# Kernel tuning notes

Hardware: AMD Instinct MI355X
Metric: run time of the kernel (lower is better)

The kernel has to match this reference:

```python
import jax, jax.numpy as jnp
import numpy as np

C1, C2, BIG_K, STRIDE = 256, 256, 13, 1
EPS = 1e-5  # BatchNorm2d default


def setup_inputs() -> dict:
    key = jax.random.key(0)
    k1, k2, k3, k4, k5 = jax.random.split(key, 5)
    x = jax.random.normal(k1, (16, C1, 56, 56), dtype=jnp.float32)
    # Conv2d weight: (out_ch, in_ch, kH, kW), kaiming-ish scale
    w = jax.random.normal(k2, (C2, C1, BIG_K, BIG_K), dtype=jnp.float32) * (1.0 / np.sqrt(C1 * BIG_K * BIG_K))
    gamma = jax.random.uniform(k3, (C2,), dtype=jnp.float32, minval=0.5, maxval=1.5)
    beta = jax.random.normal(k4, (C2,), dtype=jnp.float32) * 0.1
    running_mean = jnp.zeros((C2,), dtype=jnp.float32)
    running_var = jax.random.uniform(k5, (C2,), dtype=jnp.float32, minval=0.5, maxval=1.5)
    return {"x": x, "w": w, "gamma": gamma, "beta": beta,
            "running_mean": running_mean, "running_var": running_var}


def reference(x, w, gamma, beta, running_mean, running_var):
    # Dense big_k x big_k conv fallback: Conv2d(c1, c2, 13, stride=1, pad=6, bias=False)
    pad = BIG_K // 2
    y = jax.lax.conv_general_dilated(
        x, w,
        window_strides=(STRIDE, STRIDE),
        padding=[(pad, pad), (pad, pad)],
        dimension_numbers=("NCHW", "OIHW", "NCHW"),
    )
    # BatchNorm2d (inference mode: running stats)
    inv = jax.lax.rsqrt(running_var + EPS)
    y = (y - running_mean[None, :, None, None]) * (gamma * inv)[None, :, None, None] + beta[None, :, None, None]
    # SiLU activation
    return y * jax.nn.sigmoid(y)
```

## Files before the change

### kernel.cpp

```cpp
#include <hip/hip_runtime.h>
#include <hip/hip_bf16.h>

#define C1c 256
#define C2c 256
#define NBAT 16
#define HH 56
#define WW 56
#define KS 13
#define PADc 6
#define HP 68
#define NPIX (NBAT*HH*WW)
#define PIXTILES 196
#define KSTEPS2 1352

typedef __bf16 bf16;
typedef bf16 bf16x8 __attribute__((ext_vector_type(8)));
typedef float floatx4 __attribute__((ext_vector_type(4)));

#define XT_ELEMS ((size_t)NBAT*HP*HP*C1c)
#define WT_ELEMS ((size_t)KSTEPS2*256*32)

__global__ __launch_bounds__(256) void xform_x(const float* __restrict__ x,
                                               bf16* __restrict__ xT) {
  __shared__ bf16 tile[56][258];
  const int tid = threadIdx.x;
  const int n = blockIdx.x / HP;
  const int hp = blockIdx.x - n * HP;
  const int ih = hp - PADc;
  const size_t pos_base = (size_t)(n * HP + hp) * HP * C1c;

  if (ih < 0 || ih >= HH) {
#pragma unroll 1
    for (int i = tid; i < HP * 32; i += 256) {
      int wp = i >> 5, g = i & 31;
      *(uint4*)(xT + pos_base + wp * C1c + g * 8) = (uint4){0u, 0u, 0u, 0u};
    }
    return;
  }

  const int wave = tid >> 6, lane = tid & 63;
#pragma unroll 4
  for (int i = 0; i < 64; ++i) {
    int c = i * 4 + wave;
    if (lane < WW) {
      float v = x[(((size_t)n * C1c + c) * HH + ih) * WW + lane];
      tile[lane][c] = (bf16)v;
    }
  }
  __syncthreads();

#pragma unroll 1
  for (int i = tid; i < HP * 32; i += 256) {
    int wp = i >> 5, g = i & 31;
    int iw = wp - PADc;
    uint4 o;
    if (iw >= 0 && iw < WW) {
      const uint* lp = (const uint*)&tile[iw][g * 8];
      o.x = lp[0]; o.y = lp[1]; o.z = lp[2]; o.w = lp[3];
    } else {
      o = (uint4){0u, 0u, 0u, 0u};
    }
    *(uint4*)(xT + pos_base + wp * C1c + g * 8) = o;
  }
}

__global__ __launch_bounds__(256) void xform_w(const float* __restrict__ w,
                                               bf16* __restrict__ wT) {
  int j = blockIdx.x * 256 + threadIdx.x;
  int part = j & 3;
  int c2 = (j >> 2) & 255;
  int kk = j >> 10;
  int kw = kk % 13;
  int t = kk / 13;
  int q = t & 7;
  int kh = t >> 3;
  int c1 = q * 32 + part * 8;
  const float* wp = w + ((size_t)c2 * C1c + c1) * (KS * KS) + kh * KS + kw;
  bf16x8 v;
#pragma unroll
  for (int i = 0; i < 8; i++) v[i] = (bf16)wp[(size_t)i * KS * KS];
  *(bf16x8*)(wT + (size_t)j * 8) = v;
}

__device__ __forceinline__ void gload_lds16(const bf16* g, bf16* l) {
  __builtin_amdgcn_global_load_lds(
      (const __attribute__((address_space(1))) void*)(g),
      (__attribute__((address_space(3))) void*)(l),
      16, 0, 0);
}

__global__ __launch_bounds__(512, 2) void conv_mfma(
    const bf16* __restrict__ xT, const bf16* __restrict__ wT,
    const float* __restrict__ gamma, const float* __restrict__ beta,
    const float* __restrict__ rmean, const float* __restrict__ rvar,
    float* __restrict__ out) {
  __shared__ __attribute__((aligned(16))) bf16 As[3][256 * 32];
  __shared__ __attribute__((aligned(16))) bf16 Bs[3][256 * 32];
  __shared__ float sS[256];
  __shared__ float sB[256];

  const int tid = threadIdx.x;
  const int lane = tid & 63;
  const int wave = tid >> 6;
  const int wm = wave >> 2, wn = wave & 3;

  const int orig = blockIdx.x;
  const int xcd = orig & 7, kb = orig >> 3;
  const int pixt = (xcd < 4 ? xcd * 25 : 100 + (xcd - 4) * 24) + kb;
  const int pixbase = pixt * 256;

  if (tid < 256) {
    float s = gamma[tid] * rsqrtf(rvar[tid] + 1e-5f);
    sS[tid] = s;
    sB[tid] = beta[tid] - rmean[tid] * s;
  }
  __syncthreads();

  const int part = tid & 3;
  const int row0 = tid >> 2;
  const int srcg = (part ^ ((row0 >> 1) & 3)) * 8;

  const int aOff0 = row0 * 32 + srcg;
  const int aOff1 = aOff0 + 128 * 32;

  int pOff0, pOff1;
  {
    int pix = pixbase + row0;
    int n = pix / (HH * WW);
    int rr = pix - n * (HH * WW);
    int oh = rr / WW;
    int ow = rr - oh * WW;
    pOff0 = ((n * HP + oh) * HP + ow) * C1c + srcg;
    pix += 128;
    n = pix / (HH * WW);
    rr = pix - n * (HH * WW);
    oh = rr / WW;
    ow = rr - oh * WW;
    pOff1 = ((n * HP + oh) * HP + ow) * C1c + srcg;
  }

  const int ldsA0 = wave * 512;

  const int mrow = lane & 15;
  const int kq = lane >> 4;
  const int g0 = (kq ^ ((mrow >> 1) & 3)) * 8;
  const int aRB = (wm * 128 + mrow) * 32 + g0;
  const int bRB = (wn * 64 + mrow) * 32 + g0;

  floatx4 acc[8][4];
#pragma unroll
  for (int mi = 0; mi < 8; mi++)
#pragma unroll
    for (int ni = 0; ni < 4; ni++) acc[mi][ni] = (floatx4){0.f, 0.f, 0.f, 0.f};

  gload_lds16(wT + aOff0, &As[0][ldsA0]);
  gload_lds16(wT + aOff1, &As[0][4096 + ldsA0]);
  gload_lds16(xT + pOff0, &Bs[0][ldsA0]);
  gload_lds16(xT + pOff1, &Bs[0][4096 + ldsA0]);
  gload_lds16(wT + 8192 + aOff0, &As[1][ldsA0]);
  gload_lds16(wT + 8192 + aOff1, &As[1][4096 + ldsA0]);
  gload_lds16(xT + pOff0 + C1c, &Bs[1][ldsA0]);
  gload_lds16(xT + pOff1 + C1c, &Bs[1][4096 + ldsA0]);

  int kwn = 2, qn = 0, khn = 0;
  const bf16* aPre = wT + 2 * 8192;

  auto do_step = [&](const bf16* Ac, const bf16* Bc, bf16* An, bf16* Bn) {
    asm volatile("s_waitcnt vmcnt(4)" ::: "memory");
    __builtin_amdgcn_s_barrier();

    bf16x8 af[8], bfr[4];
#pragma unroll
    for (int mi = 0; mi < 4; mi++)
      af[mi] = *(const bf16x8*)(Ac + aRB + mi * 512);
#pragma unroll
    for (int ni = 0; ni < 4; ni++)
      bfr[ni] = *(const bf16x8*)(Bc + bRB + ni * 512);

    gload_lds16(aPre + aOff0, An + ldsA0);
    gload_lds16(aPre + aOff1, An + 4096 + ldsA0);

    __builtin_amdgcn_s_setprio(1);
#pragma unroll
    for (int mi = 0; mi < 4; mi++)
#pragma unroll
      for (int ni = 0; ni < 4; ni++)
        acc[mi][ni] = __builtin_amdgcn_mfma_f32_16x16x32_bf16(
            af[mi], bfr[ni], acc[mi][ni], 0, 0, 0);
    __builtin_amdgcn_s_setprio(0);
    __builtin_amdgcn_s_barrier();

#pragma unroll
    for (int mi = 4; mi < 8; mi++)
      af[mi] = *(const bf16x8*)(Ac + aRB + mi * 512);

    int bOn = (khn * HP + kwn) * C1c + qn * 32;
    gload_lds16(xT + pOff0 + bOn, Bn + ldsA0);
    gload_lds16(xT + pOff1 + bOn, Bn + 4096 + ldsA0);

    kwn++; aPre += 8192;
    if (kwn == 13) {
      kwn = 0; qn++;
      if (qn == 8) {
        qn = 0; khn++;
        if (khn == 13) { khn = 0; aPre = wT; }
      }
    }

    __builtin_amdgcn_s_setprio(1);
#pragma unroll
    for (int mi = 4; mi < 8; mi++)
#pragma unroll
      for (int ni = 0; ni < 4; ni++)
        acc[mi][ni] = __builtin_amdgcn_mfma_f32_16x16x32_bf16(
            af[mi], bfr[ni], acc[mi][ni], 0, 0, 0);
    __builtin_amdgcn_s_setprio(0);
  };

#pragma unroll 1
  for (int kk = 0; kk < KSTEPS2 - 2; kk += 3) {
    do_step(As[0], Bs[0], As[2], Bs[2]);
    do_step(As[1], Bs[1], As[0], Bs[0]);
    do_step(As[2], Bs[2], As[1], Bs[1]);
  }
  do_step(As[0], Bs[0], As[2], Bs[2]);
  do_step(As[1], Bs[1], As[0], Bs[0]);

  const int colL = lane & 15;
  const int quad = lane >> 4;
#pragma unroll
  for (int ni = 0; ni < 4; ni++) {
    int pix = pixbase + wn * 64 + ni * 16 + colL;
    int n = pix / (HH * WW);
    int rr = pix - n * (HH * WW);
    int oh = rr / WW;
    int ow = rr - oh * WW;
    size_t obase = (size_t)n * C2c * (HH * WW) + (size_t)oh * WW + ow;
#pragma unroll
    for (int mi = 0; mi < 8; mi++) {
      int rowb = wm * 128 + mi * 16 + quad * 4;
#pragma unroll
      for (int r = 0; r < 4; r++) {
        int rowl = rowb + r;
        float v = acc[mi][ni][r];
        v = v * sS[rowl] + sB[rowl];
        float o = v / (1.f + __expf(-v));
        out[obase + (size_t)rowl * (HH * WW)] = o;
      }
    }
  }
}

extern "C" void kernel_launch(void* const* d_in, const int* in_sizes, int n_in,
                              void* d_out, int out_size, void* d_ws, size_t ws_size,
                              hipStream_t stream) {
  const float* x     = (const float*)d_in[0];
  const float* w     = (const float*)d_in[1];
  const float* gamma = (const float*)d_in[2];
  const float* beta  = (const float*)d_in[3];
  const float* rmean = (const float*)d_in[4];
  const float* rvar  = (const float*)d_in[5];
  float* out = (float*)d_out;

  bf16* xT = (bf16*)d_ws;
  bf16* wT = xT + XT_ELEMS;

  if (ws_size < (XT_ELEMS + WT_ELEMS) * sizeof(bf16)) return;

  xform_x<<<NBAT * HP, 256, 0, stream>>>(x, xT);
  xform_w<<<(KSTEPS2 * 256 * 4) / 256, 256, 0, stream>>>(w, wT);
  conv_mfma<<<PIXTILES, 512, 0, stream>>>(xT, wT, gamma, beta, rmean, rvar, out);
}
```

Measured before the change: 1.234 ms.

## Switch conv GEMM to 32x32x16 MFMA tiles and restructure barrier placement

```diff
diff --git a/kernel.cpp b/kernel.cpp
--- a/kernel.cpp
+++ b/kernel.cpp
@@ -16,6 +16,7 @@
 typedef __bf16 bf16;
 typedef bf16 bf16x8 __attribute__((ext_vector_type(8)));
 typedef float floatx4 __attribute__((ext_vector_type(4)));
+typedef float floatx16 __attribute__((ext_vector_type(16)));
 
 #define XT_ELEMS ((size_t)NBAT*HP*HP*C1c)
 #define WT_ELEMS ((size_t)KSTEPS2*256*32)
@@ -141,17 +142,21 @@
 
   const int ldsA0 = wave * 512;
 
-  const int mrow = lane & 15;
-  const int kq = lane >> 4;
-  const int g0 = (kq ^ ((mrow >> 1) & 3)) * 8;
-  const int aRB = (wm * 128 + mrow) * 32 + g0;
-  const int bRB = (wn * 64 + mrow) * 32 + g0;
-
-  floatx4 acc[8][4];
-#pragma unroll
-  for (int mi = 0; mi < 8; mi++)
-#pragma unroll
-    for (int ni = 0; ni < 4; ni++) acc[mi][ni] = (floatx4){0.f, 0.f, 0.f, 0.f};
+  const int mrow = lane & 31;
+  const int kg = lane >> 5;
+  const int sw = (mrow >> 1) & 3;
+  const int g0 = ((kg)     ^ sw) * 8;
+  const int g1 = ((kg + 2) ^ sw) * 8;
+  const int aRB = (wm * 128 + mrow) * 32;
+  const int bRB = (wn * 64 + mrow) * 32;
+
+  floatx16 acc[4][2];
+#pragma unroll
+  for (int mi = 0; mi < 4; mi++)
+#pragma unroll
+    for (int ni = 0; ni < 2; ni++)
+#pragma unroll
+      for (int r = 0; r < 16; r++) acc[mi][ni][r] = 0.f;
 
   gload_lds16(wT + aOff0, &As[0][ldsA0]);
   gload_lds16(wT + aOff1, &As[0][4096 + ldsA0]);
@@ -161,43 +166,45 @@
   gload_lds16(wT + 8192 + aOff1, &As[1][4096 + ldsA0]);
   gload_lds16(xT + pOff0 + C1c, &Bs[1][ldsA0]);
   gload_lds16(xT + pOff1 + C1c, &Bs[1][4096 + ldsA0]);
+  asm volatile("s_waitcnt vmcnt(4)" ::: "memory");
+  __builtin_amdgcn_s_barrier();
 
   int kwn = 2, qn = 0, khn = 0;
   const bf16* aPre = wT + 2 * 8192;
 
   auto do_step = [&](const bf16* Ac, const bf16* Bc, bf16* An, bf16* Bn) {
-    asm volatile("s_waitcnt vmcnt(4)" ::: "memory");
-    __builtin_amdgcn_s_barrier();
-
-    bf16x8 af[8], bfr[4];
-#pragma unroll
-    for (int mi = 0; mi < 4; mi++)
-      af[mi] = *(const bf16x8*)(Ac + aRB + mi * 512);
-#pragma unroll
-    for (int ni = 0; ni < 4; ni++)
-      bfr[ni] = *(const bf16x8*)(Bc + bRB + ni * 512);
-
+
+    bf16x8 a0[4], b0[2];
+#pragma unroll
+    for (int mi = 0; mi < 4; mi++)
+      a0[mi] = *(const bf16x8*)(Ac + aRB + mi * 1024 + g0);
+#pragma unroll
+    for (int ni = 0; ni < 2; ni++)
+      b0[ni] = *(const bf16x8*)(Bc + bRB + ni * 1024 + g0);
     gload_lds16(aPre + aOff0, An + ldsA0);
     gload_lds16(aPre + aOff1, An + 4096 + ldsA0);
-
+    __builtin_amdgcn_sched_barrier(0);
+    __builtin_amdgcn_s_barrier();
     __builtin_amdgcn_s_setprio(1);
 #pragma unroll
     for (int mi = 0; mi < 4; mi++)
 #pragma unroll
-      for (int ni = 0; ni < 4; ni++)
-        acc[mi][ni] = __builtin_amdgcn_mfma_f32_16x16x32_bf16(
-            af[mi], bfr[ni], acc[mi][ni], 0, 0, 0);
+      for (int ni = 0; ni < 2; ni++)
+        acc[mi][ni] = __builtin_amdgcn_mfma_f32_32x32x16_bf16(
+            a0[mi], b0[ni], acc[mi][ni], 0, 0, 0);
     __builtin_amdgcn_s_setprio(0);
     __builtin_amdgcn_s_barrier();
 
-#pragma unroll
-    for (int mi = 4; mi < 8; mi++)
-      af[mi] = *(const bf16x8*)(Ac + aRB + mi * 512);
-
+    bf16x8 a1[4], b1[2];
+#pragma unroll
+    for (int mi = 0; mi < 4; mi++)
+      a1[mi] = *(const bf16x8*)(Ac + aRB + mi * 1024 + g1);
+#pragma unroll
+    for (int ni = 0; ni < 2; ni++)
+      b1[ni] = *(const bf16x8*)(Bc + bRB + ni * 1024 + g1);
     int bOn = (khn * HP + kwn) * C1c + qn * 32;
     gload_lds16(xT + pOff0 + bOn, Bn + ldsA0);
     gload_lds16(xT + pOff1 + bOn, Bn + 4096 + ldsA0);
-
     kwn++; aPre += 8192;
     if (kwn == 13) {
       kwn = 0; qn++;
@@ -206,15 +213,18 @@
         if (khn == 13) { khn = 0; aPre = wT; }
       }
     }
-
+    __builtin_amdgcn_sched_barrier(0);
+    __builtin_amdgcn_s_barrier();
     __builtin_amdgcn_s_setprio(1);
 #pragma unroll
-    for (int mi = 4; mi < 8; mi++)
-#pragma unroll
-      for (int ni = 0; ni < 4; ni++)
-        acc[mi][ni] = __builtin_amdgcn_mfma_f32_16x16x32_bf16(
-            af[mi], bfr[ni], acc[mi][ni], 0, 0, 0);
+    for (int mi = 0; mi < 4; mi++)
+#pragma unroll
+      for (int ni = 0; ni < 2; ni++)
+        acc[mi][ni] = __builtin_amdgcn_mfma_f32_32x32x16_bf16(
+            a1[mi], b1[ni], acc[mi][ni], 0, 0, 0);
     __builtin_amdgcn_s_setprio(0);
+    asm volatile("s_waitcnt vmcnt(4)" ::: "memory");
+    __builtin_amdgcn_s_barrier();
   };
 
 #pragma unroll 1
@@ -226,23 +236,20 @@
   do_step(As[0], Bs[0], As[2], Bs[2]);
   do_step(As[1], Bs[1], As[0], Bs[0]);
 
-  const int colL = lane & 15;
-  const int quad = lane >> 4;
-#pragma unroll
-  for (int ni = 0; ni < 4; ni++) {
-    int pix = pixbase + wn * 64 + ni * 16 + colL;
+  const int colp = lane & 31;
+  const int hi = lane >> 5;
+#pragma unroll
+  for (int ni = 0; ni < 2; ni++) {
+    int pix = pixbase + wn * 64 + ni * 32 + colp;
     int n = pix / (HH * WW);
     int rr = pix - n * (HH * WW);
-    int oh = rr / WW;
-    int ow = rr - oh * WW;
-    size_t obase = (size_t)n * C2c * (HH * WW) + (size_t)oh * WW + ow;
-#pragma unroll
-    for (int mi = 0; mi < 8; mi++) {
-      int rowb = wm * 128 + mi * 16 + quad * 4;
-#pragma unroll
-      for (int r = 0; r < 4; r++) {
-        int rowl = rowb + r;
-        float v = acc[mi][ni][r];
+    size_t obase = (size_t)n * C2c * (HH * WW) + rr;
+#pragma unroll
+    for (int mi = 0; mi < 4; mi++) {
+#pragma unroll
+      for (int reg = 0; reg < 16; reg++) {
+        int rowl = wm * 128 + mi * 32 + (reg & 3) + 8 * (reg >> 2) + 4 * hi;
+        float v = acc[mi][ni][reg];
         v = v * sS[rowl] + sB[rowl];
         float o = v / (1.f + __expf(-v));
         out[obase + (size_t)rowl * (HH * WW)] = o;
```

Measured after the change: 1.456 ms. 1.18x slower.

## Use 4 waves with 128x128 warp tiles and register double-buffered fragments

Applied to the files above, without the earlier changes.

```diff
diff --git a/kernel.cpp b/kernel.cpp
--- a/kernel.cpp
+++ b/kernel.cpp
@@ -89,27 +89,27 @@
       16, 0, 0);
 }
 
-__global__ __launch_bounds__(512, 2) void conv_mfma(
+__global__ __launch_bounds__(256, 1) void conv_mfma(
     const bf16* __restrict__ xT, const bf16* __restrict__ wT,
     const float* __restrict__ gamma, const float* __restrict__ beta,
     const float* __restrict__ rmean, const float* __restrict__ rvar,
     float* __restrict__ out) {
-  __shared__ __attribute__((aligned(16))) bf16 As[3][256 * 32];
-  __shared__ __attribute__((aligned(16))) bf16 Bs[3][256 * 32];
+  __shared__ __attribute__((aligned(16))) bf16 As[4][256 * 32];
+  __shared__ __attribute__((aligned(16))) bf16 Bs[4][256 * 32];
   __shared__ float sS[256];
   __shared__ float sB[256];
 
   const int tid = threadIdx.x;
   const int lane = tid & 63;
   const int wave = tid >> 6;
-  const int wm = wave >> 2, wn = wave & 3;
+  const int wm = wave >> 1, wn = wave & 1;
 
   const int orig = blockIdx.x;
   const int xcd = orig & 7, kb = orig >> 3;
   const int pixt = (xcd < 4 ? xcd * 25 : 100 + (xcd - 4) * 24) + kb;
   const int pixbase = pixt * 256;
 
-  if (tid < 256) {
+  {
     float s = gamma[tid] * rsqrtf(rvar[tid] + 1e-5f);
     sS[tid] = s;
     sB[tid] = beta[tid] - rmean[tid] * s;
@@ -120,84 +120,69 @@
   const int row0 = tid >> 2;
   const int srcg = (part ^ ((row0 >> 1) & 3)) * 8;
 
-  const int aOff0 = row0 * 32 + srcg;
-  const int aOff1 = aOff0 + 128 * 32;
-
-  int pOff0, pOff1;
-  {
-    int pix = pixbase + row0;
+  int aOffs[4];
+#pragma unroll
+  for (int i = 0; i < 4; i++) aOffs[i] = (i * 64 + row0) * 32 + srcg;
+
+  int pOffs[4];
+#pragma unroll
+  for (int i = 0; i < 4; i++) {
+    int pix = pixbase + i * 64 + row0;
     int n = pix / (HH * WW);
     int rr = pix - n * (HH * WW);
     int oh = rr / WW;
     int ow = rr - oh * WW;
-    pOff0 = ((n * HP + oh) * HP + ow) * C1c + srcg;
-    pix += 128;
-    n = pix / (HH * WW);
-    rr = pix - n * (HH * WW);
-    oh = rr / WW;
-    ow = rr - oh * WW;
-    pOff1 = ((n * HP + oh) * HP + ow) * C1c + srcg;
-  }
-
-  const int ldsA0 = wave * 512;
+    pOffs[i] = ((n * HP + oh) * HP + ow) * C1c + srcg;
+  }
+
+  const int ldsW = wave * 512;
 
   const int mrow = lane & 15;
   const int kq = lane >> 4;
   const int g0 = (kq ^ ((mrow >> 1) & 3)) * 8;
   const int aRB = (wm * 128 + mrow) * 32 + g0;
-  const int bRB = (wn * 64 + mrow) * 32 + g0;
-
-  floatx4 acc[8][4];
+  const int bRB = (wn * 128 + mrow) * 32 + g0;
+
+  floatx4 acc[8][8];
 #pragma unroll
   for (int mi = 0; mi < 8; mi++)
 #pragma unroll
-    for (int ni = 0; ni < 4; ni++) acc[mi][ni] = (floatx4){0.f, 0.f, 0.f, 0.f};
-
-  gload_lds16(wT + aOff0, &As[0][ldsA0]);
-  gload_lds16(wT + aOff1, &As[0][4096 + ldsA0]);
-  gload_lds16(xT + pOff0, &Bs[0][ldsA0]);
-  gload_lds16(xT + pOff1, &Bs[0][4096 + ldsA0]);
-  gload_lds16(wT + 8192 + aOff0, &As[1][ldsA0]);
-  gload_lds16(wT + 8192 + aOff1, &As[1][4096 + ldsA0]);
-  gload_lds16(xT + pOff0 + C1c, &Bs[1][ldsA0]);
-  gload_lds16(xT + pOff1 + C1c, &Bs[1][4096 + ldsA0]);
-
-  int kwn = 2, qn = 0, khn = 0;
-  const bf16* aPre = wT + 2 * 8192;
-
-  auto do_step = [&](const bf16* Ac, const bf16* Bc, bf16* An, bf16* Bn) {
-    asm volatile("s_waitcnt vmcnt(4)" ::: "memory");
-    __builtin_amdgcn_s_barrier();
-
-    bf16x8 af[8], bfr[4];
-#pragma unroll
-    for (int mi = 0; mi < 4; mi++)
-      af[mi] = *(const bf16x8*)(Ac + aRB + mi * 512);
-#pragma unroll
-    for (int ni = 0; ni < 4; ni++)
-      bfr[ni] = *(const bf16x8*)(Bc + bRB + ni * 512);
-
-    gload_lds16(aPre + aOff0, An + ldsA0);
-    gload_lds16(aPre + aOff1, An + 4096 + ldsA0);
-
-    __builtin_amdgcn_s_setprio(1);
-#pragma unroll
-    for (int mi = 0; mi < 4; mi++)
-#pragma unroll
-      for (int ni = 0; ni < 4; ni++)
-        acc[mi][ni] = __builtin_amdgcn_mfma_f32_16x16x32_bf16(
-            af[mi], bfr[ni], acc[mi][ni], 0, 0, 0);
-    __builtin_amdgcn_s_setprio(0);
-    __builtin_amdgcn_s_barrier();
-
-#pragma unroll
-    for (int mi = 4; mi < 8; mi++)
-      af[mi] = *(const bf16x8*)(Ac + aRB + mi * 512);
-
+    for (int ni = 0; ni < 8; ni++) acc[mi][ni] = (floatx4){0.f, 0.f, 0.f, 0.f};
+
+#pragma unroll
+  for (int s = 0; s < 3; s++) {
+#pragma unroll
+    for (int i = 0; i < 4; i++)
+      gload_lds16(wT + s * 8192 + aOffs[i], &As[s][i * 2048 + ldsW]);
+#pragma unroll
+    for (int i = 0; i < 4; i++)
+      gload_lds16(xT + pOffs[i] + s * C1c, &Bs[s][i * 2048 + ldsW]);
+  }
+  asm volatile("s_waitcnt vmcnt(8)" ::: "memory");
+  __builtin_amdgcn_s_barrier();
+
+  int kwn = 3, qn = 0, khn = 0;
+  const bf16* aPre = wT + 3 * 8192;
+
+  bf16x8 afA[8], bfA[8], afB[8], bfB[8];
+#pragma unroll
+  for (int mi = 0; mi < 8; mi++)
+    afA[mi] = *(const bf16x8*)(As[0] + aRB + mi * 512);
+#pragma unroll
+  for (int ni = 0; ni < 8; ni++)
+    bfA[ni] = *(const bf16x8*)(Bs[0] + bRB + ni * 512);
+
+  auto do_step = [&](bf16x8 (&afC)[8], bf16x8 (&bfC)[8],
+                     bf16x8 (&afN)[8], bf16x8 (&bfN)[8],
+                     const bf16* Arb, const bf16* Brb,
+                     bf16* Awb, bf16* Bwb) {
+#pragma unroll
+    for (int i = 0; i < 4; i++)
+      gload_lds16(aPre + aOffs[i], Awb + i * 2048 + ldsW);
     int bOn = (khn * HP + kwn) * C1c + qn * 32;
-    gload_lds16(xT + pOff0 + bOn, Bn + ldsA0);
-    gload_lds16(xT + pOff1 + bOn, Bn + 4096 + ldsA0);
-
+#pragma unroll
+    for (int i = 0; i < 4; i++)
+      gload_lds16(xT + pOffs[i] + bOn, Bwb + i * 2048 + ldsW);
     kwn++; aPre += 8192;
     if (kwn == 13) {
       kwn = 0; qn++;
@@ -206,31 +191,38 @@
         if (khn == 13) { khn = 0; aPre = wT; }
       }
     }
-
+#pragma unroll
+    for (int mi = 0; mi < 8; mi++)
+      afN[mi] = *(const bf16x8*)(Arb + aRB + mi * 512);
+#pragma unroll
+    for (int ni = 0; ni < 8; ni++)
+      bfN[ni] = *(const bf16x8*)(Brb + bRB + ni * 512);
+    __builtin_amdgcn_sched_barrier(0);
     __builtin_amdgcn_s_setprio(1);
 #pragma unroll
-    for (int mi = 4; mi < 8; mi++)
-#pragma unroll
-      for (int ni = 0; ni < 4; ni++)
+    for (int mi = 0; mi < 8; mi++)
+#pragma unroll
+      for (int ni = 0; ni < 8; ni++)
         acc[mi][ni] = __builtin_amdgcn_mfma_f32_16x16x32_bf16(
-            af[mi], bfr[ni], acc[mi][ni], 0, 0, 0);
+            afC[mi], bfC[ni], acc[mi][ni], 0, 0, 0);
     __builtin_amdgcn_s_setprio(0);
+    asm volatile("s_waitcnt vmcnt(8)" ::: "memory");
+    __builtin_amdgcn_s_barrier();
   };
 
 #pragma unroll 1
-  for (int kk = 0; kk < KSTEPS2 - 2; kk += 3) {
-    do_step(As[0], Bs[0], As[2], Bs[2]);
-    do_step(As[1], Bs[1], As[0], Bs[0]);
-    do_step(As[2], Bs[2], As[1], Bs[1]);
-  }
-  do_step(As[0], Bs[0], As[2], Bs[2]);
-  do_step(As[1], Bs[1], As[0], Bs[0]);
+  for (int kk = 0; kk < KSTEPS2; kk += 4) {
+    do_step(afA, bfA, afB, bfB, As[1], Bs[1], As[3], Bs[3]);
+    do_step(afB, bfB, afA, bfA, As[2], Bs[2], As[0], Bs[0]);
+    do_step(afA, bfA, afB, bfB, As[3], Bs[3], As[1], Bs[1]);
+    do_step(afB, bfB, afA, bfA, As[0], Bs[0], As[2], Bs[2]);
+  }
 
   const int colL = lane & 15;
   const int quad = lane >> 4;
 #pragma unroll
-  for (int ni = 0; ni < 4; ni++) {
-    int pix = pixbase + wn * 64 + ni * 16 + colL;
+  for (int ni = 0; ni < 8; ni++) {
+    int pix = pixbase + wn * 128 + ni * 16 + colL;
     int n = pix / (HH * WW);
     int rr = pix - n * (HH * WW);
     int oh = rr / WW;
@@ -269,5 +261,5 @@
 
   xform_x<<<NBAT * HP, 256, 0, stream>>>(x, xT);
   xform_w<<<(KSTEPS2 * 256 * 4) / 256, 256, 0, stream>>>(w, wT);
-  conv_mfma<<<PIXTILES, 512, 0, stream>>>(xT, wT, gamma, beta, rmean, rvar, out);
-}
+  conv_mfma<<<PIXTILES, 256, 0, stream>>>(xT, wT, gamma, beta, rmean, rvar, out);
+}
```

Result: slower. 2.806 ms (+127.4%).

## Load conv weight fragments directly into registers, bypassing LDS staging

Applied to the files above, without the earlier changes.

```diff
diff --git a/kernel.cpp b/kernel.cpp
--- a/kernel.cpp
+++ b/kernel.cpp
@@ -94,7 +94,6 @@
     const float* __restrict__ gamma, const float* __restrict__ beta,
     const float* __restrict__ rmean, const float* __restrict__ rvar,
     float* __restrict__ out) {
-  __shared__ __attribute__((aligned(16))) bf16 As[3][256 * 32];
   __shared__ __attribute__((aligned(16))) bf16 Bs[3][256 * 32];
   __shared__ float sS[256];
   __shared__ float sB[256];
@@ -119,9 +118,6 @@
   const int part = tid & 3;
   const int row0 = tid >> 2;
   const int srcg = (part ^ ((row0 >> 1) & 3)) * 8;
-
-  const int aOff0 = row0 * 32 + srcg;
-  const int aOff1 = aOff0 + 128 * 32;
 
   int pOff0, pOff1;
   {
@@ -144,8 +140,8 @@
   const int mrow = lane & 15;
   const int kq = lane >> 4;
   const int g0 = (kq ^ ((mrow >> 1) & 3)) * 8;
-  const int aRB = (wm * 128 + mrow) * 32 + g0;
   const int bRB = (wn * 64 + mrow) * 32 + g0;
+  const int aLane = (wm * 128 + mrow) * 32 + kq * 8;
 
   floatx4 acc[8][4];
 #pragma unroll
@@ -153,78 +149,73 @@
 #pragma unroll
     for (int ni = 0; ni < 4; ni++) acc[mi][ni] = (floatx4){0.f, 0.f, 0.f, 0.f};
 
-  gload_lds16(wT + aOff0, &As[0][ldsA0]);
-  gload_lds16(wT + aOff1, &As[0][4096 + ldsA0]);
   gload_lds16(xT + pOff0, &Bs[0][ldsA0]);
   gload_lds16(xT + pOff1, &Bs[0][4096 + ldsA0]);
-  gload_lds16(wT + 8192 + aOff0, &As[1][ldsA0]);
-  gload_lds16(wT + 8192 + aOff1, &As[1][4096 + ldsA0]);
   gload_lds16(xT + pOff0 + C1c, &Bs[1][ldsA0]);
   gload_lds16(xT + pOff1 + C1c, &Bs[1][4096 + ldsA0]);
 
+  bf16x8 afA[8], afB[8];
+#pragma unroll
+  for (int mi = 0; mi < 8; mi++)
+    afA[mi] = *(const bf16x8*)(wT + aLane + mi * 512);
+
+  asm volatile("s_waitcnt vmcnt(10)" ::: "memory");
+  __builtin_amdgcn_s_barrier();
+
   int kwn = 2, qn = 0, khn = 0;
-  const bf16* aPre = wT + 2 * 8192;
-
-  auto do_step = [&](const bf16* Ac, const bf16* Bc, bf16* An, bf16* Bn) {
-    asm volatile("s_waitcnt vmcnt(4)" ::: "memory");
-    __builtin_amdgcn_s_barrier();
-
-    bf16x8 af[8], bfr[4];
-#pragma unroll
-    for (int mi = 0; mi < 4; mi++)
-      af[mi] = *(const bf16x8*)(Ac + aRB + mi * 512);
-#pragma unroll
-    for (int ni = 0; ni < 4; ni++)
-      bfr[ni] = *(const bf16x8*)(Bc + bRB + ni * 512);
-
-    gload_lds16(aPre + aOff0, An + ldsA0);
-    gload_lds16(aPre + aOff1, An + 4096 + ldsA0);
-
-    __builtin_amdgcn_s_setprio(1);
-#pragma unroll
-    for (int mi = 0; mi < 4; mi++)
-#pragma unroll
-      for (int ni = 0; ni < 4; ni++)
-        acc[mi][ni] = __builtin_amdgcn_mfma_f32_16x16x32_bf16(
-            af[mi], bfr[ni], acc[mi][ni], 0, 0, 0);
-    __builtin_amdgcn_s_setprio(0);
-    __builtin_amdgcn_s_barrier();
-
-#pragma unroll
-    for (int mi = 4; mi < 8; mi++)
-      af[mi] = *(const bf16x8*)(Ac + aRB + mi * 512);
+  const bf16* aPreF = wT + 8192;
+  int slabA = 1;
+
+  auto do_step = [&](bf16x8 (&afC)[8], bf16x8 (&afN)[8],
+                     const bf16* Bc, bf16* Bwb) {
+#pragma unroll
+    for (int mi = 0; mi < 8; mi++)
+      afN[mi] = *(const bf16x8*)(aPreF + aLane + mi * 512);
+    aPreF += 8192;
+    if (++slabA == KSTEPS2) { slabA = 0; aPreF = wT; }
 
     int bOn = (khn * HP + kwn) * C1c + qn * 32;
-    gload_lds16(xT + pOff0 + bOn, Bn + ldsA0);
-    gload_lds16(xT + pOff1 + bOn, Bn + 4096 + ldsA0);
-
-    kwn++; aPre += 8192;
+    gload_lds16(xT + pOff0 + bOn, Bwb + ldsA0);
+    gload_lds16(xT + pOff1 + bOn, Bwb + 4096 + ldsA0);
+    kwn++;
     if (kwn == 13) {
       kwn = 0; qn++;
       if (qn == 8) {
         qn = 0; khn++;
-        if (khn == 13) { khn = 0; aPre = wT; }
+        if (khn == 13) khn = 0;
       }
     }
 
+    bf16x8 bfr[4];
+#pragma unroll
+    for (int ni = 0; ni < 4; ni++)
+      bfr[ni] = *(const bf16x8*)(Bc + bRB + ni * 512);
+    __builtin_amdgcn_sched_barrier(0);
+
     __builtin_amdgcn_s_setprio(1);
 #pragma unroll
-    for (int mi = 4; mi < 8; mi++)
+    for (int mi = 0; mi < 8; mi++)
 #pragma unroll
       for (int ni = 0; ni < 4; ni++)
         acc[mi][ni] = __builtin_amdgcn_mfma_f32_16x16x32_bf16(
-            af[mi], bfr[ni], acc[mi][ni], 0, 0, 0);
+            afC[mi], bfr[ni], acc[mi][ni], 0, 0, 0);
     __builtin_amdgcn_s_setprio(0);
+
+    asm volatile("s_waitcnt vmcnt(10)" ::: "memory");
+    __builtin_amdgcn_s_barrier();
   };
 
 #pragma unroll 1
-  for (int kk = 0; kk < KSTEPS2 - 2; kk += 3) {
-    do_step(As[0], Bs[0], As[2], Bs[2]);
-    do_step(As[1], Bs[1], As[0], Bs[0]);
-    do_step(As[2], Bs[2], As[1], Bs[1]);
-  }
-  do_step(As[0], Bs[0], As[2], Bs[2]);
-  do_step(As[1], Bs[1], As[0], Bs[0]);
+  for (int kk = 0; kk < KSTEPS2 - 2; kk += 6) {
+    do_step(afA, afB, Bs[0], Bs[2]);
+    do_step(afB, afA, Bs[1], Bs[0]);
+    do_step(afA, afB, Bs[2], Bs[1]);
+    do_step(afB, afA, Bs[0], Bs[2]);
+    do_step(afA, afB, Bs[1], Bs[0]);
+    do_step(afB, afA, Bs[2], Bs[1]);
+  }
+  do_step(afA, afB, Bs[0], Bs[2]);
+  do_step(afB, afA, Bs[1], Bs[0]);
 
   const int colL = lane & 15;
   const int quad = lane >> 4;
```

Measured after the change: 2.511 ms. 2.03x slower.
